# Kernel optimization log

Hardware: AMD Instinct MI355X
Metric: run time of the kernel (lower is better)

The kernel has to match this reference:

```python
import jax, jax.numpy as jnp
import numpy as np

B, L, C, H = 1, 2048, 2048, 16
D = C // H
EPS = 1e-6
W0 = 30.0  # SIREN frequency

def rmsnorm(x, w, eps=EPS):
    return x * jax.lax.rsqrt(jnp.mean(x * x, axis=-1, keepdims=True) + eps) * w

def depth_rope(x, depth, base=10000.0):
    # same rotation for all positions, angle set by scalar layer depth
    d = x.shape[-1]
    half = d // 2
    freqs = 1.0 / base ** (jnp.arange(half, dtype=x.dtype) / half)
    ang = depth * freqs
    cos, sin = jnp.cos(ang), jnp.sin(ang)
    x1, x2 = x[..., :half], x[..., half:2 * half]
    return jnp.concatenate([x1 * cos - x2 * sin, x1 * sin + x2 * cos], axis=-1)

def setup_inputs() -> dict:
    key = jax.random.key(0)
    ks = jax.random.split(key, 13)
    s = 1.0 / np.sqrt(C)
    inp = {
        'x':  jax.random.normal(ks[0], (B, L, C), jnp.float32),
        'h0': jax.random.normal(ks[1], (B, L, C), jnp.float32),
        'h1': jax.random.normal(ks[2], (B, L, C), jnp.float32),
        'h2': jax.random.normal(ks[3], (B, L, C), jnp.float32),
        'Wq': jax.random.normal(ks[4], (C, C), jnp.float32) * s,
        'Wk': jax.random.normal(ks[5], (C, C), jnp.float32) * s,
        'Wv': jax.random.normal(ks[6], (C, C), jnp.float32) * s,
        'Wo': jax.random.normal(ks[7], (C, C), jnp.float32) * s,
        'qn_w': jnp.ones((D,), jnp.float32),
        'kn_w': jnp.ones((D,), jnp.float32),
        'on_w': jnp.ones((C,), jnp.float32),
        'sw1': jax.random.normal(ks[8], (1, C), jnp.float32),
        'sb1': jax.random.normal(ks[9], (C,), jnp.float32) * 0.01,
        'sw2': jax.random.normal(ks[10], (C, C), jnp.float32) * s,
        'sb2': jnp.zeros((C,), jnp.float32),
    }
    return inp

def reference(x, h0, h1, h2, Wq, Wk, Wv, Wo, qn_w, kn_w, on_w, sw1, sb1, sw2, sb2):
    history = [h0, h1, h2]
    q_src = history[-1]                      # [B,L,C]
    q_depth = len(history) - 1
    # Q path: proj -> per-head RMSNorm -> depth RoPE
    q = jnp.einsum('blc,oc->blo', q_src, Wq).reshape(B, L, H, D)
    q = depth_rope(rmsnorm(q, qn_w), q_depth)
    # K/V path over prior history entries (each with its own depth)
    k_parts, v_parts = [], []
    for depth_idx, kv in enumerate(history[:-1]):
        k_i = jnp.einsum('blc,oc->blo', kv, Wk).reshape(B, L, H, D)
        v_i = jnp.einsum('blc,oc->blo', kv, Wv).reshape(B, L, H, D)
        k_parts.append(depth_rope(rmsnorm(k_i, kn_w), depth_idx))
        v_parts.append(v_i)
    k = jnp.concatenate(k_parts, axis=1)     # [B,Lkv,H,D]
    v = jnp.concatenate(v_parts, axis=1)
    # full SDPA, default scale D^-0.5
    scores = jnp.einsum('bqhd,bkhd->bhqk', q, k) * (D ** -0.5)
    attn = jax.nn.softmax(scores, axis=-1)
    out = jnp.einsum('bhqk,bkhd->bqhd', attn, v).reshape(B, L, C)
    out = jnp.einsum('blc,oc->blo', out, Wo)
    # SIREN upsample to (L,): target length == L -> identity interpolation
    # plus sine-activated coordinate MLP (implicit positional field)
    coords = jnp.linspace(-1.0, 1.0, L, dtype=x.dtype)[:, None]   # [L,1]
    pos = jnp.sin(W0 * (coords @ sw1 + sb1)) @ sw2 + sb2           # [L,C]
    out = out + pos[None]
    return x + rmsnorm(out, on_w)
```

## Files before the change

### kernel.cpp

```cpp
#include <hip/hip_runtime.h>
#include <hip/hip_fp16.h>

#define LQ 2048
#define CDIM 2048
#define NHEAD 16
#define HDIM 128
#define LKEY 4096

typedef _Float16 f16x8 __attribute__((ext_vector_type(8)));
typedef _Float16 f16x4 __attribute__((ext_vector_type(4)));
typedef float f32x4 __attribute__((ext_vector_type(4)));

#define GLOAD_LDS16(g, s) __builtin_amdgcn_global_load_lds( \
    (const __attribute__((address_space(1))) void*)(g),     \
    (__attribute__((address_space(3))) void*)(s), 16, 0, 0)

#define MFMA16(a, b, c) __builtin_amdgcn_mfma_f32_16x16x32_f16(a, b, c, 0, 0, 0)

__device__ __forceinline__ void storeC(float* p, float v) { *p = v; }
__device__ __forceinline__ void storeC(__half* p, float v) { *p = __float2half(v); }

template <int MODE, typename OutT>
__device__ __forceinline__ void gemm_body(
    __half* smem,
    const __half* __restrict__ A, const __half* __restrict__ B,
    OutT* __restrict__ C, int lda, int ldb, int ldc, int K,
    int bmA, int bmC, int bn,
    const float* __restrict__ wgt, int kmode, float oscale)
{
    __half* lA = smem;
    __half* lB = smem + 8192;
    const int tid  = threadIdx.x;
    const int lane = tid & 63;
    const int wave = tid >> 6;
    const int r = tid >> 3;
    const int g = tid & 7;
    const __half* gA = A + (long)(bmA * 128 + r) * lda + ((g ^ (r & 7)) << 3);
    const __half* gB = B + (long)(bn * 128 + r) * ldb + ((g ^ (r & 7)) << 3);
    __half* lAp = lA + tid * 8;
    __half* lBp = lB + tid * 8;
    const int wr = (wave & 1) << 6;
    const int wc = (wave >> 1) << 6;
    const int l15 = lane & 15, quad = lane >> 4;

    f32x4 acc[4][4] = {};

    for (int kt = 0; kt < K; kt += 64) {
#pragma unroll
        for (int i = 0; i < 4; ++i) {
            GLOAD_LDS16(gA + (long)i * 32 * lda, lAp + i * 2048);
            GLOAD_LDS16(gB + (long)i * 32 * ldb, lBp + i * 2048);
        }
        gA += 64; gB += 64;
        __syncthreads();
#pragma unroll
        for (int kk = 0; kk < 2; ++kk) {
            f16x8 af[4], bfr[4];
#pragma unroll
            for (int mi = 0; mi < 4; ++mi) {
                const int m = wr + mi * 16 + l15;
                const int kg = kk * 4 + quad;
                af[mi] = *(const f16x8*)&lA[m * 64 + ((kg ^ (m & 7)) << 3)];
            }
#pragma unroll
            for (int ni = 0; ni < 4; ++ni) {
                const int n = wc + ni * 16 + l15;
                const int kg = kk * 4 + quad;
                bfr[ni] = *(const f16x8*)&lB[n * 64 + ((kg ^ (n & 7)) << 3)];
            }
#pragma unroll
            for (int mi = 0; mi < 4; ++mi)
#pragma unroll
                for (int ni = 0; ni < 4; ++ni)
                    acc[mi][ni] = MFMA16(af[mi], bfr[ni], acc[mi][ni]);
        }
        __syncthreads();
    }

    if constexpr (MODE == 0) {
        const int row0 = bmC * 128 + wr + quad * 4;
        const int col0 = bn * 128 + wc + l15;
#pragma unroll
        for (int mi = 0; mi < 4; ++mi)
#pragma unroll
            for (int ni = 0; ni < 4; ++ni)
#pragma unroll
                for (int rx = 0; rx < 4; ++rx)
                    storeC(&C[(long)(row0 + mi * 16 + rx) * ldc + col0 + ni * 16],
                           acc[mi][ni][rx]);
    } else {
        __half* sT = smem;
#pragma unroll
        for (int mi = 0; mi < 4; ++mi)
#pragma unroll
            for (int ni = 0; ni < 4; ++ni)
#pragma unroll
                for (int rx = 0; rx < 4; ++rx)
                    sT[(wr + mi * 16 + quad * 4 + rx) * 136 + wc + ni * 16 + l15] =
                        (_Float16)acc[mi][ni][rx];
        __syncthreads();
        const int row = (wave << 5) + (lane >> 1);
        const int c0  = (lane & 1) << 5;
        const __half* rp = sT + row * 136;
        f16x8 L[4], Hh[4];
#pragma unroll
        for (int j8 = 0; j8 < 4; ++j8) {
            L[j8]  = *(const f16x8*)&rp[c0 + j8 * 8];
            Hh[j8] = *(const f16x8*)&rp[c0 + 64 + j8 * 8];
        }
        float ss = 0.f;
#pragma unroll
        for (int j8 = 0; j8 < 4; ++j8)
#pragma unroll
            for (int e = 0; e < 8; ++e) {
                const float a = (float)L[j8][e], b = (float)Hh[j8][e];
                ss += a * a + b * b;
            }
        ss += __shfl_xor(ss, 1);
        const float rn = rsqrtf(ss * (1.0f / 128.0f) + 1e-6f);
        const long grow = (long)bmC * 128 + row;
        const int depth = kmode ? (grow < 2048 ? 0 : 1) : 2;
        union { f16x8 v; _Float16 e[8]; } o1[4], o2[4];
#pragma unroll
        for (int j8 = 0; j8 < 4; ++j8)
#pragma unroll
            for (int e = 0; e < 8; ++e) {
                const int d = c0 + j8 * 8 + e;
                const float x1 = (float)L[j8][e]  * rn * wgt[d];
                const float x2 = (float)Hh[j8][e] * rn * wgt[d + 64];
                const float ang = (float)depth *
                    exp2f(-(float)d * 0.20762050593045702f);
                float sn, cs;
                __sincosf(ang, &sn, &cs);
                o1[j8].e[e] = (_Float16)((x1 * cs - x2 * sn) * oscale);
                o2[j8].e[e] = (_Float16)((x1 * sn + x2 * cs) * oscale);
            }
        __half* op = (__half*)C + grow * ldc + bn * 128;
#pragma unroll
        for (int j8 = 0; j8 < 4; ++j8) {
            *(f16x8*)&op[c0 + j8 * 8]      = o1[j8].v;
            *(f16x8*)&op[c0 + 64 + j8 * 8] = o2[j8].v;
        }
    }
}

__device__ __forceinline__ void stage_half(
    const __half* __restrict__ M, long row0, int T, char* lds, int slot, int tid)
{
    char* dst = lds + slot * 16384 + tid * 16;
    const int r = tid >> 3;
    const int g = tid & 7;
    const int co = T * 64 + ((g ^ (r & 7)) << 3);
    GLOAD_LDS16(M + (row0 + r) * 2048 + co, dst);
    GLOAD_LDS16(M + (row0 + r + 64) * 2048 + co, dst + 8192);
}

__global__ __launch_bounds__(512, 1) void gemm_kv8(
    const __half* __restrict__ A,
    const __half* __restrict__ B,
    __half* __restrict__ Ckv,
    __half* __restrict__ vT,
    const float* __restrict__ kn_w)
{
    __shared__ __align__(16) char LDS[131072];
    const int tid  = threadIdx.x;
    const int lane = tid & 63;
    const int wave = tid >> 6;
    const int wm = wave >> 2;
    const int wn = wave & 3;
    const int l15 = lane & 15, quad = lane >> 4;
    const int bm = blockIdx.x & 15;
    const int bn = blockIdx.x >> 4;
    const long arow = (long)bm * 256;
    const long brow = (long)bn * 256;

    f32x4 acc[8][4] = {};

    stage_half(A, arow,       0, LDS, 0, tid);
    stage_half(A, arow + 128, 0, LDS, 1, tid);
    stage_half(B, brow,       0, LDS, 4, tid);
    stage_half(B, brow + 128, 0, LDS, 5, tid);

    for (int tt = 0; tt < 32; ++tt) {
        const int buf = tt & 1, sbuf = buf ^ 1;
        const int Tn = (tt < 31) ? tt + 1 : 31;
        const __half* As = (const __half*)(LDS + (buf * 2 + wm) * 16384);
        const __half* Bs = (const __half*)(LDS + (4 + buf * 2 + (wn >> 1)) * 16384);
        f16x8 bq[4][2];
#pragma unroll
        for (int q = 0; q < 4; ++q) {
            if (q == 0)      stage_half(A, arow,       Tn, LDS, 0 + sbuf * 2, tid);
            else if (q == 1) stage_half(A, arow + 128, Tn, LDS, 1 + sbuf * 2, tid);
            else if (q == 2) stage_half(B, brow,       Tn, LDS, 4 + sbuf * 2, tid);
            else             stage_half(B, brow + 128, Tn, LDS, 5 + sbuf * 2, tid);
            if (q == 0)
                asm volatile("s_waitcnt vmcnt(2)" ::: "memory");
            __builtin_amdgcn_s_barrier();
            __builtin_amdgcn_sched_barrier(0);
            if (q == 0) {
#pragma unroll
                for (int ni = 0; ni < 4; ++ni) {
                    const int rb = ((wn & 1) << 6) + ni * 16 + l15;
#pragma unroll
                    for (int ks = 0; ks < 2; ++ks)
                        bq[ni][ks] = *(const f16x8*)
                            &Bs[rb * 64 + (((ks * 4 + quad) ^ (rb & 7)) << 3)];
                }
            }
            f16x8 av[2][2];
#pragma unroll
            for (int m2 = 0; m2 < 2; ++m2) {
                const int ra = (q * 2 + m2) * 16 + l15;
#pragma unroll
                for (int ks = 0; ks < 2; ++ks)
                    av[m2][ks] = *(const f16x8*)
                        &As[ra * 64 + (((ks * 4 + quad) ^ (ra & 7)) << 3)];
            }
            __builtin_amdgcn_s_setprio(1);
#pragma unroll
            for (int m2 = 0; m2 < 2; ++m2)
#pragma unroll
                for (int ni = 0; ni < 4; ++ni) {
                    acc[q * 2 + m2][ni] = MFMA16(av[m2][0], bq[ni][0], acc[q * 2 + m2][ni]);
                    acc[q * 2 + m2][ni] = MFMA16(av[m2][1], bq[ni][1], acc[q * 2 + m2][ni]);
                }
            __builtin_amdgcn_s_setprio(0);
            __builtin_amdgcn_s_barrier();
            __builtin_amdgcn_sched_barrier(0);
        }
    }

    __syncthreads();

    if (bn < 8) {
        __half* sT = (__half*)LDS;
#pragma unroll
        for (int mi = 0; mi < 8; ++mi)
#pragma unroll
            for (int ni = 0; ni < 4; ++ni)
#pragma unroll
                for (int rx = 0; rx < 4; ++rx)
                    sT[(wm * 128 + mi * 16 + quad * 4 + rx) * 256 +
                       wn * 64 + ni * 16 + l15] = (_Float16)acc[mi][ni][rx];
        __syncthreads();
        const int row = tid >> 1;
        const int hs  = tid & 1;
        const __half* rp = sT + row * 256 + hs * 128;
        f16x8 xv[16];
#pragma unroll
        for (int j = 0; j < 16; ++j) xv[j] = *(const f16x8*)&rp[j * 8];
        float ss = 0.f;
#pragma unroll
        for (int j = 0; j < 16; ++j)
#pragma unroll
            for (int e = 0; e < 8; ++e) {
                const float v = (float)xv[j][e];
                ss += v * v;
            }
        const float rn = rsqrtf(ss * (1.0f / 128.0f) + 1e-6f);
        const long R = arow + row;
        const float depth = (R < 2048) ? 0.f : 1.f;
        __half* op = Ckv + R * 4096 + bn * 256 + hs * 128;
#pragma unroll
        for (int j = 0; j < 8; ++j) {
            union { f16x8 v; _Float16 e[8]; } o1, o2;
#pragma unroll
            for (int e = 0; e < 8; ++e) {
                const int d = j * 8 + e;
                const float x1 = (float)xv[j][e]     * rn * kn_w[d];
                const float x2 = (float)xv[j + 8][e] * rn * kn_w[d + 64];
                const float ang = depth * exp2f(-(float)d * 0.20762050593045702f);
                float sn, cs;
                __sincosf(ang, &sn, &cs);
                o1.e[e] = (_Float16)(x1 * cs - x2 * sn);
                o2.e[e] = (_Float16)(x1 * sn + x2 * cs);
            }
            *(f16x8*)&op[j * 8]      = o1.v;
            *(f16x8*)&op[64 + j * 8] = o2.v;
        }
    } else {
#pragma unroll
        for (int mi = 0; mi < 8; ++mi)
#pragma unroll
            for (int ni = 0; ni < 4; ++ni)
#pragma unroll
                for (int rx = 0; rx < 4; ++rx) {
                    const int d = (bn - 8) * 256 + wn * 64 + ni * 16 + l15;
                    const long key = arow + wm * 128 + mi * 16 + quad * 4 + rx;
                    vT[(long)d * LKEY + key] = __float2half(acc[mi][ni][rx]);
                }
    }
}

__global__ __launch_bounds__(256, 2) void gemm_q(
    const __half* __restrict__ A, const __half* __restrict__ Bq,
    __half* __restrict__ Cq, const float* __restrict__ qn_w)
{
    __shared__ __align__(16) __half smem[17408];
    const int bm = blockIdx.x & 15, bn = blockIdx.x >> 4;
    gemm_body<1, __half>(smem, A, Bq, Cq, 2048, 2048, 2048, 2048,
                         bm, bm, bn, qn_w, 0, 0.12751743f);
}

__global__ __launch_bounds__(256, 2) void gemm_sk(
    const __half* __restrict__ A, const __half* __restrict__ B,
    float* __restrict__ C, int lda, int ldb, int ldc, int Khalf)
{
    __shared__ __align__(16) __half smem[16384];
    const int z = blockIdx.z;
    gemm_body<0, float>(smem, A + z * Khalf, B + z * Khalf,
                        C + (long)z * LQ * CDIM,
                        lda, ldb, ldc, Khalf, blockIdx.x, blockIdx.x, blockIdx.y,
                        nullptr, 0, 1.0f);
}

__global__ __launch_bounds__(256, 2) void attn_tile(
    const __half* __restrict__ Qf,
    const __half* __restrict__ Kf,
    const __half* __restrict__ Vt,
    float* __restrict__ Opart,
    float* __restrict__ lsum)
{
    __shared__ __align__(16) __half lK[64 * 128];
    __shared__ __align__(16) __half lV[128 * 64];
    __shared__ __align__(16) __half pL[4 * 2 * 16 * 76];

    const int tid  = threadIdx.x;
    const int lane = tid & 63;
    const int wave = tid >> 6;
    const int l15  = lane & 15;
    const int quad = lane >> 4;
    const int lin = blockIdx.y * 16 + blockIdx.x;
    const int hkc = (lin & 7) * 4 + ((lin >> 3) & 3);
    const int qt  = lin >> 5;
    const int h   = hkc >> 1;
    const int kc  = hkc & 1;
    const int q0  = qt * 128 + wave * 32;

    f16x8 aq[2][4];
#pragma unroll
    for (int mt = 0; mt < 2; ++mt)
#pragma unroll
        for (int ks = 0; ks < 4; ++ks)
            aq[mt][ks] = *(const f16x8*)&Qf[(long)(q0 + mt * 16 + l15) * CDIM +
                                            h * HDIM + ks * 32 + quad * 8];

    const int rK = tid >> 4;
    const int gK = tid & 15;
    const __half* srcK = Kf + (long)(kc * 2048 + rK) * 4096 + h * HDIM +
                         ((gK ^ (rK & 15)) << 3);
    const int rV = tid >> 3;
    const int gV = tid & 7;
    const __half* srcV = Vt + (long)(h * HDIM + rV) * (long)LKEY + kc * 2048 +
                         ((gV ^ (rV & 7)) << 3);
    __half* dstK = lK + tid * 8;
    __half* dstV = lV + tid * 8;

    f32x4 accO[2][8] = {};
    f32x4 l_acc[2] = {};

    for (int st = 0; st < 32; ++st) {
#pragma unroll
        for (int i = 0; i < 4; ++i) {
            GLOAD_LDS16(srcK + (long)(st * 64 + i * 16) * 4096, dstK + i * 2048);
            GLOAD_LDS16(srcV + (long)i * 32 * LKEY + st * 64, dstV + i * 2048);
        }
        __syncthreads();
        f32x4 s[2][4];
#pragma unroll
        for (int mt = 0; mt < 2; ++mt)
#pragma unroll
            for (int nt = 0; nt < 4; ++nt)
                s[mt][nt] = (f32x4){-10.f, -10.f, -10.f, -10.f};
#pragma unroll
        for (int nt = 0; nt < 4; ++nt) {
            const int n = nt * 16 + l15;
#pragma unroll
            for (int ks = 0; ks < 4; ++ks) {
                const f16x8 kf = *(const f16x8*)
                    &lK[n * 128 + (((ks * 4 + quad) ^ (n & 15)) << 3)];
                s[0][nt] = MFMA16(aq[0][ks], kf, s[0][nt]);
                s[1][nt] = MFMA16(aq[1][ks], kf, s[1][nt]);
            }
        }
#pragma unroll
        for (int mt = 0; mt < 2; ++mt)
#pragma unroll
            for (int nt = 0; nt < 4; ++nt)
#pragma unroll
                for (int r2 = 0; r2 < 4; ++r2) {
                    const float p = __builtin_amdgcn_exp2f(s[mt][nt][r2]);
                    l_acc[mt][r2] += p;
                    pL[((wave * 2 + mt) * 16 + quad * 4 + r2) * 76 +
                       nt * 16 + l15] = __float2half(p);
                }
        f16x8 ap[2][2];
#pragma unroll
        for (int mt = 0; mt < 2; ++mt) {
            ap[mt][0] = *(const f16x8*)&pL[((wave * 2 + mt) * 16 + l15) * 76 + quad * 8];
            ap[mt][1] = *(const f16x8*)&pL[((wave * 2 + mt) * 16 + l15) * 76 + 32 + quad * 8];
        }
#pragma unroll
        for (int nt2 = 0; nt2 < 8; ++nt2) {
            const int n2 = nt2 * 16 + l15;
            const f16x8 v0 = *(const f16x8*)&lV[n2 * 64 + ((quad ^ (n2 & 7)) << 3)];
            const f16x8 v1 = *(const f16x8*)&lV[n2 * 64 + (((4 + quad) ^ (n2 & 7)) << 3)];
            accO[0][nt2] = MFMA16(ap[0][0], v0, accO[0][nt2]);
            accO[0][nt2] = MFMA16(ap[0][1], v1, accO[0][nt2]);
            accO[1][nt2] = MFMA16(ap[1][0], v0, accO[1][nt2]);
            accO[1][nt2] = MFMA16(ap[1][1], v1, accO[1][nt2]);
        }
        __syncthreads();
    }

#pragma unroll
    for (int mt = 0; mt < 2; ++mt)
#pragma unroll
        for (int r2 = 0; r2 < 4; ++r2) {
            float v = l_acc[mt][r2];
            v += __shfl_xor(v, 1);
            v += __shfl_xor(v, 2);
            v += __shfl_xor(v, 4);
            v += __shfl_xor(v, 8);
            if (l15 == 0)
                atomicAdd(&lsum[h * LQ + q0 + mt * 16 + quad * 4 + r2], v);
        }
    float* Cp = Opart + (long)kc * LQ * CDIM + h * HDIM;
#pragma unroll
    for (int mt = 0; mt < 2; ++mt)
#pragma unroll
        for (int nt2 = 0; nt2 < 8; ++nt2)
#pragma unroll
            for (int rx = 0; rx < 4; ++rx)
                Cp[(long)(q0 + mt * 16 + quad * 4 + rx) * CDIM + nt2 * 16 + l15] =
                    accO[mt][nt2][rx];
}

__global__ __launch_bounds__(256) void merge_o(
    const float* __restrict__ Op, const float* __restrict__ lsum,
    __half* __restrict__ a2)
{
    const int row = blockIdx.x;
    const int c0  = threadIdx.x * 8;
    const float inv = 1.0f / lsum[(c0 >> 7) * LQ + row];
    const float* p0 = Op + (long)row * CDIM + c0;
    const float* p1 = p0 + (long)LQ * CDIM;
    union { f16x8 v; _Float16 e[8]; } o;
#pragma unroll
    for (int j = 0; j < 8; ++j)
        o.e[j] = (_Float16)((p0[j] + p1[j]) * inv);
    *(f16x8*)&a2[(long)row * 4096 + c0] = o.v;
}

__global__ __launch_bounds__(256) void prep_all(
    const float* __restrict__ h2, const float* __restrict__ h0,
    const float* __restrict__ h1, const float* __restrict__ Wq,
    const float* __restrict__ Wk, const float* __restrict__ Wv,
    const float* __restrict__ Wo, const float* __restrict__ sw1,
    const float* __restrict__ sb1, const float* __restrict__ sw2,
    __half* __restrict__ xq, __half* __restrict__ xkv,
    __half* __restrict__ wqh, __half* __restrict__ wkv,
    __half* __restrict__ a2, __half* __restrict__ b2,
    float* __restrict__ lsum)
{
    __shared__ float t[64][65];
    const int blk = blockIdx.x;
    const int tid = threadIdx.x;
    if (blk < 24576) {
        const long i = ((long)blk * 256 + tid) << 2;
        const int chunk = (int)(i >> 22);
        const long off = i & 4194303;
        const float* s; __half* d;
        switch (chunk) {
            case 0:  s = h2; d = xq;            break;
            case 1:  s = h0; d = xkv;           break;
            case 2:  s = h1; d = xkv + 4194304; break;
            case 3:  s = Wq; d = wqh;           break;
            case 4:  s = Wk; d = wkv;           break;
            default: s = Wv; d = wkv + 4194304; break;
        }
        const float4 v = *(const float4*)&s[off];
        f16x4 o;
        o[0] = (_Float16)v.x; o[1] = (_Float16)v.y;
        o[2] = (_Float16)v.z; o[3] = (_Float16)v.w;
        *(f16x4*)&d[off] = o;
    } else if (blk < 28672) {
        const int i = ((blk - 24576) * 256 + tid) << 2;
        const int o = i >> 11, c = i & 2047;
        const float4 v = *(const float4*)&Wo[i];
        f16x4 w4;
        w4[0] = (_Float16)v.x; w4[1] = (_Float16)v.y;
        w4[2] = (_Float16)v.z; w4[3] = (_Float16)v.w;
        *(f16x4*)&b2[((long)o << 12) + c] = w4;
    } else if (blk < 29696) {
        const int lb = blk - 28672;
        const long r0 = (long)(lb & 31) * 64;
        const long c0 = (long)(lb >> 5) * 64;
        const int tj = tid & 63;
        const int ti = tid >> 6;
#pragma unroll
        for (int it = 0; it < 16; ++it) {
            const int i = it * 4 + ti;
            t[i][tj] = sw2[(r0 + i) * 2048 + c0 + tj];
        }
        __syncthreads();
#pragma unroll
        for (int it = 0; it < 16; ++it) {
            const int i = it * 4 + ti;
            b2[(c0 + i) * 4096 + 2048 + r0 + tj] = __float2half(t[tj][i]);
        }
    } else if (blk < 33792) {
        const int i = ((blk - 29696) * 256 + tid) << 2;
        const int l = i >> 11, c = i & 2047;
        const float coord = -1.0f + (2.0f / 2047.0f) * (float)l;
        const float4 w = *(const float4*)&sw1[c];
        const float4 b = *(const float4*)&sb1[c];
        f16x4 o;
        o[0] = (_Float16)__sinf(30.0f * (coord * w.x + b.x));
        o[1] = (_Float16)__sinf(30.0f * (coord * w.y + b.y));
        o[2] = (_Float16)__sinf(30.0f * (coord * w.z + b.z));
        o[3] = (_Float16)__sinf(30.0f * (coord * w.w + b.w));
        *(f16x4*)&a2[((long)l << 12) + 2048 + c] = o;
    } else {
        const int i = ((blk - 33792) * 256 + tid) << 2;
        *(float4*)&lsum[i] = (float4){0.f, 0.f, 0.f, 0.f};
    }
}

__global__ __launch_bounds__(256) void final_norm(
    const float* __restrict__ out2, const float* __restrict__ x,
    const float* __restrict__ sb2, const float* __restrict__ on_w,
    float* __restrict__ y)
{
    const int row = blockIdx.x;
    const float* o0 = out2 + (long)row * CDIM;
    const float* o1 = o0 + (long)LQ * CDIM;
    float4 v[2];
    float ss = 0.f;
#pragma unroll
    for (int i = 0; i < 2; ++i) {
        const int c = threadIdx.x * 4 + i * 1024;
        const float4 a = *(const float4*)&o0[c];
        const float4 b = *(const float4*)&o1[c];
        const float4 s = *(const float4*)&sb2[c];
        float4 tv;
        tv.x = a.x + b.x + s.x; tv.y = a.y + b.y + s.y;
        tv.z = a.z + b.z + s.z; tv.w = a.w + b.w + s.w;
        v[i] = tv;
        ss += tv.x * tv.x + tv.y * tv.y + tv.z * tv.z + tv.w * tv.w;
    }
#pragma unroll
    for (int off = 1; off < 64; off <<= 1) ss += __shfl_xor(ss, off);
    __shared__ float red[4];
    const int lane = threadIdx.x & 63, wv = threadIdx.x >> 6;
    if (lane == 0) red[wv] = ss;
    __syncthreads();
    const float tot = red[0] + red[1] + red[2] + red[3];
    const float rn = rsqrtf(tot * (1.0f / 2048.0f) + 1e-6f);
#pragma unroll
    for (int i = 0; i < 2; ++i) {
        const int c = threadIdx.x * 4 + i * 1024;
        const float4 xr = *(const float4*)&x[(long)row * CDIM + c];
        const float4 wv4 = *(const float4*)&on_w[c];
        float4 o;
        o.x = xr.x + v[i].x * rn * wv4.x;
        o.y = xr.y + v[i].y * rn * wv4.y;
        o.z = xr.z + v[i].z * rn * wv4.z;
        o.w = xr.w + v[i].w * rn * wv4.w;
        *(float4*)&y[(long)row * CDIM + c] = o;
    }
}

extern "C" void kernel_launch(void* const* d_in, const int* in_sizes, int n_in,
                              void* d_out, int out_size, void* d_ws, size_t ws_size,
                              hipStream_t stream) {
    const float* x    = (const float*)d_in[0];
    const float* h0   = (const float*)d_in[1];
    const float* h1   = (const float*)d_in[2];
    const float* h2   = (const float*)d_in[3];
    const float* Wq   = (const float*)d_in[4];
    const float* Wk   = (const float*)d_in[5];
    const float* Wv   = (const float*)d_in[6];
    const float* Wo   = (const float*)d_in[7];
    const float* qn_w = (const float*)d_in[8];
    const float* kn_w = (const float*)d_in[9];
    const float* on_w = (const float*)d_in[10];
    const float* sw1  = (const float*)d_in[11];
    const float* sb1  = (const float*)d_in[12];
    const float* sw2  = (const float*)d_in[13];
    const float* sb2  = (const float*)d_in[14];
    float* y = (float*)d_out;

    const size_t MB = 1ull << 20;
    char* w = (char*)d_ws;
    __half* xq  = (__half*)(w);
    __half* xkv = (__half*)(w + 8 * MB);
    __half* wqh = (__half*)(w + 24 * MB);
    __half* wkv = (__half*)(w + 32 * MB);
    __half* qf  = (__half*)(w + 48 * MB);
    __half* kvf = (__half*)(w + 56 * MB);
    __half* vT  = (__half*)(w + 88 * MB);
    __half* a2  = (__half*)(w + 104 * MB);
    __half* b2  = (__half*)(w + 120 * MB);
    float* lsum  = (float*)(w + 136 * MB);
    float* Opart = (float*)(w);
    float* out2  = (float*)(w);
    (void)in_sizes; (void)n_in; (void)out_size; (void)ws_size;

    prep_all<<<33824, 256, 0, stream>>>(h2, h0, h1, Wq, Wk, Wv, Wo, sw1, sb1,
                                        sw2, xq, xkv, wqh, wkv, a2, b2, lsum);

    gemm_kv8<<<256, 512, 0, stream>>>(xkv, wkv, kvf, vT, kn_w);
    gemm_q<<<256, 256, 0, stream>>>(xq, wqh, qf, qn_w);

    attn_tile<<<dim3(16, 32), 256, 0, stream>>>(qf, kvf, vT, Opart, lsum);
    merge_o<<<2048, 256, 0, stream>>>(Opart, lsum, a2);

    gemm_sk<<<dim3(16, 16, 2), 256, 0, stream>>>(a2, b2, out2, 4096, 4096, 2048, 2048);
    final_norm<<<2048, 256, 0, stream>>>(out2, x, sb2, on_w, y);
}
```

Baseline: 435.6 us.

## Split-K the Q projection and move norm+RoPE into a separate kernel

The Q projection GEMM used 256 blocks with the RMSNorm and RoPE fused into its epilogue. It now uses split-K over two halves of K, giving 512 blocks, and writes fp32 partials. A new normrope_q kernel sums the partials and applies the per-head RMSNorm, depth RoPE and scale. The aim is better CU occupancy for the Q GEMM, paid for by extra fp32 traffic (two 16MB partial buffers) and one more launch.

Result: no change. 430.6 us (-1.2%).

```diff
diff --git a/kernel.cpp b/kernel.cpp
--- a/kernel.cpp
+++ b/kernel.cpp
@@ -25,8 +25,7 @@
     __half* smem,
     const __half* __restrict__ A, const __half* __restrict__ B,
     OutT* __restrict__ C, int lda, int ldb, int ldc, int K,
-    int bmA, int bmC, int bn,
-    const float* __restrict__ wgt, int kmode, float oscale)
+    int bmA, int bmC, int bn)
 {
     __half* lA = smem;
     __half* lB = smem + 8192;
@@ -77,71 +76,16 @@
         __syncthreads();
     }
 
-    if constexpr (MODE == 0) {
-        const int row0 = bmC * 128 + wr + quad * 4;
-        const int col0 = bn * 128 + wc + l15;
-#pragma unroll
-        for (int mi = 0; mi < 4; ++mi)
-#pragma unroll
-            for (int ni = 0; ni < 4; ++ni)
-#pragma unroll
-                for (int rx = 0; rx < 4; ++rx)
-                    storeC(&C[(long)(row0 + mi * 16 + rx) * ldc + col0 + ni * 16],
-                           acc[mi][ni][rx]);
-    } else {
-        __half* sT = smem;
-#pragma unroll
-        for (int mi = 0; mi < 4; ++mi)
-#pragma unroll
-            for (int ni = 0; ni < 4; ++ni)
-#pragma unroll
-                for (int rx = 0; rx < 4; ++rx)
-                    sT[(wr + mi * 16 + quad * 4 + rx) * 136 + wc + ni * 16 + l15] =
-                        (_Float16)acc[mi][ni][rx];
-        __syncthreads();
-        const int row = (wave << 5) + (lane >> 1);
-        const int c0  = (lane & 1) << 5;
-        const __half* rp = sT + row * 136;
-        f16x8 L[4], Hh[4];
-#pragma unroll
-        for (int j8 = 0; j8 < 4; ++j8) {
-            L[j8]  = *(const f16x8*)&rp[c0 + j8 * 8];
-            Hh[j8] = *(const f16x8*)&rp[c0 + 64 + j8 * 8];
-        }
-        float ss = 0.f;
-#pragma unroll
-        for (int j8 = 0; j8 < 4; ++j8)
-#pragma unroll
-            for (int e = 0; e < 8; ++e) {
-                const float a = (float)L[j8][e], b = (float)Hh[j8][e];
-                ss += a * a + b * b;
-            }
-        ss += __shfl_xor(ss, 1);
-        const float rn = rsqrtf(ss * (1.0f / 128.0f) + 1e-6f);
-        const long grow = (long)bmC * 128 + row;
-        const int depth = kmode ? (grow < 2048 ? 0 : 1) : 2;
-        union { f16x8 v; _Float16 e[8]; } o1[4], o2[4];
-#pragma unroll
-        for (int j8 = 0; j8 < 4; ++j8)
-#pragma unroll
-            for (int e = 0; e < 8; ++e) {
-                const int d = c0 + j8 * 8 + e;
-                const float x1 = (float)L[j8][e]  * rn * wgt[d];
-                const float x2 = (float)Hh[j8][e] * rn * wgt[d + 64];
-                const float ang = (float)depth *
-                    exp2f(-(float)d * 0.20762050593045702f);
-                float sn, cs;
-                __sincosf(ang, &sn, &cs);
-                o1[j8].e[e] = (_Float16)((x1 * cs - x2 * sn) * oscale);
-                o2[j8].e[e] = (_Float16)((x1 * sn + x2 * cs) * oscale);
-            }
-        __half* op = (__half*)C + grow * ldc + bn * 128;
-#pragma unroll
-        for (int j8 = 0; j8 < 4; ++j8) {
-            *(f16x8*)&op[c0 + j8 * 8]      = o1[j8].v;
-            *(f16x8*)&op[c0 + 64 + j8 * 8] = o2[j8].v;
-        }
-    }
+    const int row0 = bmC * 128 + wr + quad * 4;
+    const int col0 = bn * 128 + wc + l15;
+#pragma unroll
+    for (int mi = 0; mi < 4; ++mi)
+#pragma unroll
+        for (int ni = 0; ni < 4; ++ni)
+#pragma unroll
+            for (int rx = 0; rx < 4; ++rx)
+                storeC(&C[(long)(row0 + mi * 16 + rx) * ldc + col0 + ni * 16],
+                       acc[mi][ni][rx]);
 }
 
 __device__ __forceinline__ void stage_half(
@@ -292,14 +236,64 @@
     }
 }
 
-__global__ __launch_bounds__(256, 2) void gemm_q(
+__global__ __launch_bounds__(256, 2) void gemm_skq(
     const __half* __restrict__ A, const __half* __restrict__ Bq,
-    __half* __restrict__ Cq, const float* __restrict__ qn_w)
-{
-    __shared__ __align__(16) __half smem[17408];
-    const int bm = blockIdx.x & 15, bn = blockIdx.x >> 4;
-    gemm_body<1, __half>(smem, A, Bq, Cq, 2048, 2048, 2048, 2048,
-                         bm, bm, bn, qn_w, 0, 0.12751743f);
+    float* __restrict__ qp0, float* __restrict__ qp1)
+{
+    __shared__ __align__(16) __half smem[16384];
+    const int z = blockIdx.z;
+    float* C = z ? qp1 : qp0;
+    gemm_body<0, float>(smem, A + z * 1024, Bq + z * 1024, C,
+                        2048, 2048, 2048, 1024,
+                        blockIdx.x, blockIdx.x, blockIdx.y);
+}
+
+__global__ __launch_bounds__(256) void normrope_q(
+    const float* __restrict__ qp0, const float* __restrict__ qp1,
+    __half* __restrict__ qf, const float* __restrict__ qn_w)
+{
+    const int tid  = threadIdx.x;
+    const int row  = blockIdx.x * 2 + (tid >> 7);
+    const int head = (tid >> 3) & 15;
+    const int sub  = tid & 7;
+    const long base = (long)row * 2048 + head * 128 + sub * 8;
+
+    const float4 p0a = *(const float4*)&qp0[base];
+    const float4 p0b = *(const float4*)&qp0[base + 4];
+    const float4 p1a = *(const float4*)&qp1[base];
+    const float4 p1b = *(const float4*)&qp1[base + 4];
+    const float4 q0a = *(const float4*)&qp0[base + 64];
+    const float4 q0b = *(const float4*)&qp0[base + 68];
+    const float4 q1a = *(const float4*)&qp1[base + 64];
+    const float4 q1b = *(const float4*)&qp1[base + 68];
+    float x1[8] = {p0a.x + p1a.x, p0a.y + p1a.y, p0a.z + p1a.z, p0a.w + p1a.w,
+                   p0b.x + p1b.x, p0b.y + p1b.y, p0b.z + p1b.z, p0b.w + p1b.w};
+    float x2[8] = {q0a.x + q1a.x, q0a.y + q1a.y, q0a.z + q1a.z, q0a.w + q1a.w,
+                   q0b.x + q1b.x, q0b.y + q1b.y, q0b.z + q1b.z, q0b.w + q1b.w};
+
+    float ss = 0.f;
+#pragma unroll
+    for (int j = 0; j < 8; ++j) ss += x1[j] * x1[j] + x2[j] * x2[j];
+    ss += __shfl_xor(ss, 1);
+    ss += __shfl_xor(ss, 2);
+    ss += __shfl_xor(ss, 4);
+    const float rn = rsqrtf(ss * (1.0f / 128.0f) + 1e-6f);
+
+    union { f16x8 v; _Float16 e[8]; } o1, o2;
+#pragma unroll
+    for (int j = 0; j < 8; ++j) {
+        const int d = sub * 8 + j;
+        const float a1 = x1[j] * rn * qn_w[d];
+        const float a2 = x2[j] * rn * qn_w[d + 64];
+        const float ang = 2.0f * exp2f(-(float)d * 0.20762050593045702f);
+        float sn, cs;
+        __sincosf(ang, &sn, &cs);
+        o1.e[j] = (_Float16)((a1 * cs - a2 * sn) * 0.12751743f);
+        o2.e[j] = (_Float16)((a1 * sn + a2 * cs) * 0.12751743f);
+    }
+    __half* op = qf + base;
+    *(f16x8*)&op[0]  = o1.v;
+    *(f16x8*)&op[64] = o2.v;
 }
 
 __global__ __launch_bounds__(256, 2) void gemm_sk(
@@ -310,8 +304,7 @@
     const int z = blockIdx.z;
     gemm_body<0, float>(smem, A + z * Khalf, B + z * Khalf,
                         C + (long)z * LQ * CDIM,
-                        lda, ldb, ldc, Khalf, blockIdx.x, blockIdx.x, blockIdx.y,
-                        nullptr, 0, 1.0f);
+                        lda, ldb, ldc, Khalf, blockIdx.x, blockIdx.x, blockIdx.y);
 }
 
 __global__ __launch_bounds__(256, 2) void attn_tile(
@@ -603,6 +596,8 @@
     __half* a2  = (__half*)(w + 104 * MB);
     __half* b2  = (__half*)(w + 120 * MB);
     float* lsum  = (float*)(w + 136 * MB);
+    float* qp0   = (float*)(w + 8 * MB);
+    float* qp1   = (float*)(w + 32 * MB);
     float* Opart = (float*)(w);
     float* out2  = (float*)(w);
     (void)in_sizes; (void)n_in; (void)out_size; (void)ws_size;
@@ -611,7 +606,8 @@
                                         sw2, xq, xkv, wqh, wkv, a2, b2, lsum);
 
     gemm_kv8<<<256, 512, 0, stream>>>(xkv, wkv, kvf, vT, kn_w);
-    gemm_q<<<256, 256, 0, stream>>>(xq, wqh, qf, qn_w);
+    gemm_skq<<<dim3(16, 16, 2), 256, 0, stream>>>(xq, wqh, qp0, qp1);
+    normrope_q<<<1024, 256, 0, stream>>>(qp0, qp1, qf, qn_w);
 
     attn_tile<<<dim3(16, 32), 256, 0, stream>>>(qf, kvf, vT, Opart, lsum);
     merge_o<<<2048, 256, 0, stream>>>(Opart, lsum, a2);
```
